# Performance work log

Measured on AMD Instinct MI355X. Metric: run time of the kernel, lower is better.

Reference implementation:

```python
import jax, jax.numpy as jnp
import numpy as np

N_NODES = 100000
N_EDGES = 1600000
D_FEAT = 64
EPS = 1e-07


def setup_inputs() -> dict:
    key = jax.random.key(0)
    k1, k2, k3 = jax.random.split(key, 3)
    x = jax.random.normal(k1, (N_NODES, D_FEAT), dtype=jnp.float32)
    beta = jnp.ones((1,), dtype=jnp.float32)
    edge_row = jnp.sort(jax.random.randint(k2, (N_EDGES,), 0, N_NODES, dtype=jnp.int64))
    edge_col = jax.random.randint(k3, (N_EDGES,), 0, N_NODES, dtype=jnp.int64)
    return {"x": x, "beta": beta, "edge_row": edge_row, "edge_col": edge_col}


def reference(x, beta, edge_row, edge_col):
    # Gather endpoint features: [E, d]
    A = x[edge_row]
    B = x[edge_col]
    # Cosine similarity per edge, scaled by beta: [E]
    inner = jnp.sum(A * B, axis=1)
    norms = jnp.linalg.norm(A, axis=1) * jnp.linalg.norm(B, axis=1)
    sim = beta[0] * (inner / (norms + EPS))
    # Sparse row-wise softmax (tf.sparse.softmax): stable segment softmax over edges grouped by row
    row_max = jax.ops.segment_max(sim, edge_row, num_segments=N_NODES)
    e = jnp.exp(sim - row_max[edge_row])
    row_sum = jax.ops.segment_sum(e, edge_row, num_segments=N_NODES)
    p = e / row_sum[edge_row]  # [E]
    # SPMM: out[i] = sum_{(i,j) in E} p_ij * x[j]
    out = jax.ops.segment_sum(p[:, None] * B, edge_row, num_segments=N_NODES)
    return out
```

## Files before the change

### kernel.cpp

```cpp
#include <hip/hip_runtime.h>
#include <math.h>

#define D_FEAT 64

__global__ __launch_bounds__(256)
void agnn_rnorm(const float* __restrict__ x, float* __restrict__ rn, int n_nodes) {
    int t = blockIdx.x * blockDim.x + threadIdx.x;
    int node = t >> 4;
    if (node >= n_nodes) return;
    int l4 = t & 15;
    float4 v = ((const float4*)x)[node * 16 + l4];
    float ss = v.x * v.x + v.y * v.y + v.z * v.z + v.w * v.w;
    #pragma unroll
    for (int off = 1; off < 16; off <<= 1)
        ss += __shfl_xor(ss, off, 64);
    if (l4 == 0) rn[node] = ss > 0.f ? rsqrtf(ss) : 0.f;
}

__global__ __launch_bounds__(256)
void agnn_rowptr(const int* __restrict__ edge_row, int* __restrict__ row_ptr,
                 int n_nodes, int n_edges) {
    int e = blockIdx.x * blockDim.x + threadIdx.x;
    if (e >= n_edges) return;
    int r1 = edge_row[e];
    int r0 = (e == 0) ? -1 : edge_row[e - 1];
    for (int r = r0 + 1; r <= r1; ++r) row_ptr[r] = e;
    if (e == n_edges - 1) {
        for (int r = r1 + 1; r <= n_nodes; ++r) row_ptr[r] = n_edges;
    }
}

__global__ __launch_bounds__(256)
void agnn_fused(const float* __restrict__ x,
                const float* __restrict__ beta_p,
                const int* __restrict__ edge_col,
                const int* __restrict__ row_ptr,
                const float* __restrict__ rn,
                float* __restrict__ out, int n_nodes) {
    int node = (blockIdx.x * blockDim.x + threadIdx.x) >> 6;
    if (node >= n_nodes) return;
    int lane = threadIdx.x & 63;
    int g  = lane >> 4;
    int l4 = lane & 15;

    const float4* x4 = (const float4*)x;
    float4 xi  = x4[node * 16 + l4];
    float beta = beta_p[0];
    float brni = beta * rn[node];
    float shift = fabsf(beta);

    int es = row_ptr[node];
    int deg = row_ptr[node + 1] - es;

    float s = 0.f;
    float4 acc = {0.f, 0.f, 0.f, 0.f};

    for (int base = 0; base < deg; base += 8) {
        int ei0 = base + g;
        int ei1 = base + 4 + g;
        bool v0 = ei0 < deg;
        bool v1 = ei1 < deg;
        int ea = es + (v0 ? ei0 : 0);
        int eb = es + (v1 ? ei1 : 0);
        int c0 = edge_col[ea];
        int c1 = edge_col[eb];
        float4 a = x4[c0 * 16 + l4];
        float4 b = x4[c1 * 16 + l4];
        float rn0 = rn[c0];
        float rn1 = rn[c1];

        float d0 = a.x * xi.x + a.y * xi.y + a.z * xi.z + a.w * xi.w;
        float d1 = b.x * xi.x + b.y * xi.y + b.z * xi.z + b.w * xi.w;
        #pragma unroll
        for (int off = 1; off < 16; off <<= 1) {
            d0 += __shfl_xor(d0, off, 64);
            d1 += __shfl_xor(d1, off, 64);
        }

        float w0 = v0 ? __expf(brni * d0 * rn0 - shift) : 0.f;
        float w1 = v1 ? __expf(brni * d1 * rn1 - shift) : 0.f;
        s += w0 + w1;
        acc.x += w0 * a.x + w1 * b.x;
        acc.y += w0 * a.y + w1 * b.y;
        acc.z += w0 * a.z + w1 * b.z;
        acc.w += w0 * a.w + w1 * b.w;
    }

    #pragma unroll
    for (int off = 16; off < 64; off <<= 1) {
        s     += __shfl_xor(s,     off, 64);
        acc.x += __shfl_xor(acc.x, off, 64);
        acc.y += __shfl_xor(acc.y, off, 64);
        acc.z += __shfl_xor(acc.z, off, 64);
        acc.w += __shfl_xor(acc.w, off, 64);
    }

    if (g == 0) {
        float inv = (deg > 0 && s > 0.f) ? 1.f / s : 0.f;
        float4 o = {acc.x * inv, acc.y * inv, acc.z * inv, acc.w * inv};
        ((float4*)out)[node * 16 + l4] = o;
    }
}

extern "C" void kernel_launch(void* const* d_in, const int* in_sizes, int n_in,
                              void* d_out, int out_size, void* d_ws, size_t ws_size,
                              hipStream_t stream) {
    const float* x        = (const float*)d_in[0];
    const float* beta     = (const float*)d_in[1];
    const int*   edge_row = (const int*)d_in[2];
    const int*   edge_col = (const int*)d_in[3];
    float* out = (float*)d_out;

    int n_nodes = in_sizes[0] / D_FEAT;
    int n_edges = in_sizes[2];

    float* rn = (float*)d_ws;
    size_t rn_bytes = ((size_t)n_nodes * sizeof(float) + 255) & ~(size_t)255;
    int* row_ptr = (int*)((char*)d_ws + rn_bytes);

    {
        long long threads = (long long)n_nodes * 16;
        int blocks = (int)((threads + 255) / 256);
        agnn_rnorm<<<blocks, 256, 0, stream>>>(x, rn, n_nodes);
    }
    {
        int blocks = (n_edges + 255) / 256;
        agnn_rowptr<<<blocks, 256, 0, stream>>>(edge_row, row_ptr, n_nodes, n_edges);
    }
    {
        int blocks = (n_nodes + 3) / 4;
        agnn_fused<<<blocks, 256, 0, stream>>>(x, beta, edge_col, row_ptr, rn,
                                               out, n_nodes);
    }
}
```

Baseline: 150.3 us.

## Use fp16 MFMA tiles for per-edge scores and SpMM over 16-node tiles

Converts x to an fp16 copy during prep and merges the norm and row_ptr kernels into one launch. The main kernel now gives each wave a tile of 16 consecutive nodes and walks that tile's combined edge list 32 edges at a time. Edge similarities come from MFMA dot products, and the weighted aggregation runs as a second MFMA after staging the gathered features and weights through LDS. Gathered bytes are halved and the shuffle reductions go away, but the MFMA scores are computed against all 16 tile rows and then masked by edge_row, which wastes compute. Inputs and weights are rounded to fp16, which costs precision.

```diff
diff --git a/kernel.cpp b/kernel.cpp
--- a/kernel.cpp
+++ b/kernel.cpp
@@ -2,104 +2,220 @@
 #include <math.h>
 
 #define D_FEAT 64
+#define S_GET(v, i) ((v)[i])
+typedef _Float16 v8h __attribute__((ext_vector_type(8)));
+typedef float v4f __attribute__((ext_vector_type(4)));
+typedef _Float16 h2 __attribute__((ext_vector_type(2)));
+
+__device__ __forceinline__ v8h u2h8(uint4 u) { v8h v; __builtin_memcpy(&v, &u, 16); return v; }
 
 __global__ __launch_bounds__(256)
-void agnn_rnorm(const float* __restrict__ x, float* __restrict__ rn, int n_nodes) {
-    int t = blockIdx.x * blockDim.x + threadIdx.x;
-    int node = t >> 4;
-    if (node >= n_nodes) return;
-    int l4 = t & 15;
-    float4 v = ((const float4*)x)[node * 16 + l4];
-    float ss = v.x * v.x + v.y * v.y + v.z * v.z + v.w * v.w;
-    #pragma unroll
-    for (int off = 1; off < 16; off <<= 1)
-        ss += __shfl_xor(ss, off, 64);
-    if (l4 == 0) rn[node] = ss > 0.f ? rsqrtf(ss) : 0.f;
+void agnn_prep(const float* __restrict__ x, float* __restrict__ rn,
+               uint2* __restrict__ xh, const int* __restrict__ edge_row,
+               int* __restrict__ row_ptr, int n_nodes, int n_edges, int nb_prep) {
+    if ((int)blockIdx.x < nb_prep) {
+        int t = blockIdx.x * blockDim.x + threadIdx.x;
+        int node = t >> 4;
+        if (node >= n_nodes) return;
+        int l4 = t & 15;
+        float4 v = ((const float4*)x)[node * 16 + l4];
+        float ss = v.x*v.x + v.y*v.y + v.z*v.z + v.w*v.w;
+        #pragma unroll
+        for (int off = 1; off < 16; off <<= 1) ss += __shfl_xor(ss, off, 64);
+        if (l4 == 0) rn[node] = ss > 0.f ? rsqrtf(ss) : 0.f;
+        h2 h0 = {(_Float16)v.x, (_Float16)v.y};
+        h2 h1 = {(_Float16)v.z, (_Float16)v.w};
+        uint2 u;
+        __builtin_memcpy(&u.x, &h0, 4);
+        __builtin_memcpy(&u.y, &h1, 4);
+        xh[node * 16 + l4] = u;
+    } else {
+        int e = (blockIdx.x - nb_prep) * blockDim.x + threadIdx.x;
+        if (e >= n_edges) return;
+        int r1 = edge_row[e];
+        int r0 = (e == 0) ? -1 : edge_row[e - 1];
+        for (int r = r0 + 1; r <= r1; ++r) row_ptr[r] = e;
+        if (e == n_edges - 1)
+            for (int r = r1 + 1; r <= n_nodes; ++r) row_ptr[r] = n_edges;
+    }
 }
 
+#define XCP_PITCH 144
+#define P_PITCH    80
+#define WAVE_LDS  (32 * XCP_PITCH + 16 * P_PITCH)
+
 __global__ __launch_bounds__(256)
-void agnn_rowptr(const int* __restrict__ edge_row, int* __restrict__ row_ptr,
-                 int n_nodes, int n_edges) {
-    int e = blockIdx.x * blockDim.x + threadIdx.x;
-    if (e >= n_edges) return;
-    int r1 = edge_row[e];
-    int r0 = (e == 0) ? -1 : edge_row[e - 1];
-    for (int r = r0 + 1; r <= r1; ++r) row_ptr[r] = e;
-    if (e == n_edges - 1) {
-        for (int r = r1 + 1; r <= n_nodes; ++r) row_ptr[r] = n_edges;
-    }
-}
-
-__global__ __launch_bounds__(256)
-void agnn_fused(const float* __restrict__ x,
-                const float* __restrict__ beta_p,
+void agnn_fused(const float* __restrict__ beta_p,
                 const int* __restrict__ edge_col,
+                const int* __restrict__ edge_row,
                 const int* __restrict__ row_ptr,
                 const float* __restrict__ rn,
+                const uint4* __restrict__ xh4,
                 float* __restrict__ out, int n_nodes) {
-    int node = (blockIdx.x * blockDim.x + threadIdx.x) >> 6;
-    if (node >= n_nodes) return;
+    __shared__ char lds_raw[4 * WAVE_LDS];
+    int wid  = threadIdx.x >> 6;
     int lane = threadIdx.x & 63;
-    int g  = lane >> 4;
-    int l4 = lane & 15;
-
-    const float4* x4 = (const float4*)x;
-    float4 xi  = x4[node * 16 + l4];
-    float beta = beta_p[0];
-    float brni = beta * rn[node];
+    int q    = lane >> 4;
+    int lo4  = lane & 15;
+    char* XCP = lds_raw + wid * WAVE_LDS;
+    char* PL  = XCP + 32 * XCP_PITCH;
+
+    int tile = blockIdx.x * 4 + wid;
+    int t0 = tile * 16;
+    if (t0 >= n_nodes) return;
+
+    int qnode = t0 + lo4; if (qnode >= n_nodes) qnode = n_nodes - 1;
+    v8h a0 = u2h8(xh4[(size_t)qnode * 8 + q]);
+    v8h a1 = u2h8(xh4[(size_t)qnode * 8 + 4 + q]);
+
+    float beta  = beta_p[0];
     float shift = fabsf(beta);
-
-    int es = row_ptr[node];
-    int deg = row_ptr[node + 1] - es;
-
-    float s = 0.f;
-    float4 acc = {0.f, 0.f, 0.f, 0.f};
-
-    for (int base = 0; base < deg; base += 8) {
-        int ei0 = base + g;
-        int ei1 = base + 4 + g;
-        bool v0 = ei0 < deg;
-        bool v1 = ei1 < deg;
-        int ea = es + (v0 ? ei0 : 0);
-        int eb = es + (v1 ? ei1 : 0);
-        int c0 = edge_col[ea];
-        int c1 = edge_col[eb];
-        float4 a = x4[c0 * 16 + l4];
-        float4 b = x4[c1 * 16 + l4];
-        float rn0 = rn[c0];
-        float rn1 = rn[c1];
-
-        float d0 = a.x * xi.x + a.y * xi.y + a.z * xi.z + a.w * xi.w;
-        float d1 = b.x * xi.x + b.y * xi.y + b.z * xi.z + b.w * xi.w;
-        #pragma unroll
-        for (int off = 1; off < 16; off <<= 1) {
-            d0 += __shfl_xor(d0, off, 64);
-            d1 += __shfl_xor(d1, off, 64);
-        }
-
-        float w0 = v0 ? __expf(brni * d0 * rn0 - shift) : 0.f;
-        float w1 = v1 ? __expf(brni * d1 * rn1 - shift) : 0.f;
-        s += w0 + w1;
-        acc.x += w0 * a.x + w1 * b.x;
-        acc.y += w0 * a.y + w1 * b.y;
-        acc.z += w0 * a.z + w1 * b.z;
-        acc.w += w0 * a.w + w1 * b.w;
+    float4 rq = *(const float4*)(rn + t0 + q * 4);
+    float brn0 = beta * rq.x, brn1 = beta * rq.y, brn2 = beta * rq.z, brn3 = beta * rq.w;
+
+    int es   = row_ptr[t0];
+    int tend = t0 + 16; if (tend > n_nodes) tend = n_nodes;
+    int L    = row_ptr[tend] - es;
+
+    v4f o0 = {0,0,0,0}, o1 = {0,0,0,0}, o2 = {0,0,0,0}, o3 = {0,0,0,0};
+    float l0 = 0.f, l1 = 0.f, l2 = 0.f, l3 = 0.f;
+    unsigned int selp = (lo4 & 1) ? 0x07060302u : 0x05040100u;
+    int rbase = t0 + q * 4;
+
+    for (int base = 0; base < L; base += 32) {
+        int idx0 = base + lo4;
+        bool cv0 = idx0 < L;
+        int e0 = es + (cv0 ? idx0 : 0);
+        int c0 = edge_col[e0];
+        int rr0 = edge_row[e0];
+        float rnc0 = rn[c0];
+        uint4 u00 = xh4[(size_t)c0 * 8 + q];
+        uint4 u01 = xh4[(size_t)c0 * 8 + 4 + q];
+        int idx1 = base + 16 + lo4;
+        bool cv1 = idx1 < L;
+        int e1 = es + (cv1 ? idx1 : 0);
+        int c1 = edge_col[e1];
+        int rr1 = edge_row[e1];
+        float rnc1 = rn[c1];
+        uint4 u10 = xh4[(size_t)c1 * 8 + q];
+        uint4 u11 = xh4[(size_t)c1 * 8 + 4 + q];
+
+        v4f z0 = {0,0,0,0};
+        z0 = __builtin_amdgcn_mfma_f32_16x16x32_f16(a0, u2h8(u00), z0, 0, 0, 0);
+        z0 = __builtin_amdgcn_mfma_f32_16x16x32_f16(a1, u2h8(u01), z0, 0, 0, 0);
+        v4f z1 = {0,0,0,0};
+        z1 = __builtin_amdgcn_mfma_f32_16x16x32_f16(a0, u2h8(u10), z1, 0, 0, 0);
+        z1 = __builtin_amdgcn_mfma_f32_16x16x32_f16(a1, u2h8(u11), z1, 0, 0, 0);
+
+        {
+            unsigned int colA = lo4 * 4, colB = (16 + lo4) * 4;
+            char* pA = XCP + (4 * q) * XCP_PITCH;
+            char* pB = XCP + (16 + 4 * q) * XCP_PITCH;
+            *(unsigned int*)(pA + 0 * XCP_PITCH + colA) = u00.x;
+            *(unsigned int*)(pA + 1 * XCP_PITCH + colA) = u00.y;
+            *(unsigned int*)(pA + 2 * XCP_PITCH + colA) = u00.z;
+            *(unsigned int*)(pA + 3 * XCP_PITCH + colA) = u00.w;
+            *(unsigned int*)(pB + 0 * XCP_PITCH + colA) = u01.x;
+            *(unsigned int*)(pB + 1 * XCP_PITCH + colA) = u01.y;
+            *(unsigned int*)(pB + 2 * XCP_PITCH + colA) = u01.z;
+            *(unsigned int*)(pB + 3 * XCP_PITCH + colA) = u01.w;
+            *(unsigned int*)(pA + 0 * XCP_PITCH + colB) = u10.x;
+            *(unsigned int*)(pA + 1 * XCP_PITCH + colB) = u10.y;
+            *(unsigned int*)(pA + 2 * XCP_PITCH + colB) = u10.z;
+            *(unsigned int*)(pA + 3 * XCP_PITCH + colB) = u10.w;
+            *(unsigned int*)(pB + 0 * XCP_PITCH + colB) = u11.x;
+            *(unsigned int*)(pB + 1 * XCP_PITCH + colB) = u11.y;
+            *(unsigned int*)(pB + 2 * XCP_PITCH + colB) = u11.z;
+            *(unsigned int*)(pB + 3 * XCP_PITCH + colB) = u11.w;
+        }
+
+        float w00 = (cv0 && rr0 == rbase + 0) ? __expf(brn0 * rnc0 * z0[0] - shift) : 0.f;
+        float w01 = (cv0 && rr0 == rbase + 1) ? __expf(brn1 * rnc0 * z0[1] - shift) : 0.f;
+        float w02 = (cv0 && rr0 == rbase + 2) ? __expf(brn2 * rnc0 * z0[2] - shift) : 0.f;
+        float w03 = (cv0 && rr0 == rbase + 3) ? __expf(brn3 * rnc0 * z0[3] - shift) : 0.f;
+        float w10 = (cv1 && rr1 == rbase + 0) ? __expf(brn0 * rnc1 * z1[0] - shift) : 0.f;
+        float w11 = (cv1 && rr1 == rbase + 1) ? __expf(brn1 * rnc1 * z1[1] - shift) : 0.f;
+        float w12 = (cv1 && rr1 == rbase + 2) ? __expf(brn2 * rnc1 * z1[2] - shift) : 0.f;
+        float w13 = (cv1 && rr1 == rbase + 3) ? __expf(brn3 * rnc1 * z1[3] - shift) : 0.f;
+        l0 += w00 + w10; l1 += w01 + w11; l2 += w02 + w12; l3 += w03 + w13;
+
+        {
+            unsigned int cA = lo4 * 2, cB = (16 + lo4) * 2;
+            char* pm = PL + (q * 4) * P_PITCH;
+            *(_Float16*)(pm + 0 * P_PITCH + cA) = (_Float16)w00;
+            *(_Float16*)(pm + 1 * P_PITCH + cA) = (_Float16)w01;
+            *(_Float16*)(pm + 2 * P_PITCH + cA) = (_Float16)w02;
+            *(_Float16*)(pm + 3 * P_PITCH + cA) = (_Float16)w03;
+            *(_Float16*)(pm + 0 * P_PITCH + cB) = (_Float16)w10;
+            *(_Float16*)(pm + 1 * P_PITCH + cB) = (_Float16)w11;
+            *(_Float16*)(pm + 2 * P_PITCH + cB) = (_Float16)w12;
+            *(_Float16*)(pm + 3 * P_PITCH + cB) = (_Float16)w13;
+        }
+
+        v8h pah = u2h8(*(const uint4*)(PL + lo4 * P_PITCH + q * 16));
+        {
+            const char* rp = XCP + (0 + (lo4 >> 1)) * XCP_PITCH + q * 32;
+            uint4 da = *(const uint4*)rp;
+            uint4 db = *(const uint4*)(rp + 16);
+            uint4 bb = { __builtin_amdgcn_perm(da.y, da.x, selp),
+                         __builtin_amdgcn_perm(da.w, da.z, selp),
+                         __builtin_amdgcn_perm(db.y, db.x, selp),
+                         __builtin_amdgcn_perm(db.w, db.z, selp) };
+            o0 = __builtin_amdgcn_mfma_f32_16x16x32_f16(pah, u2h8(bb), o0, 0, 0, 0);
+        }
+        {
+            const char* rp = XCP + (8 + (lo4 >> 1)) * XCP_PITCH + q * 32;
+            uint4 da = *(const uint4*)rp;
+            uint4 db = *(const uint4*)(rp + 16);
+            uint4 bb = { __builtin_amdgcn_perm(da.y, da.x, selp),
+                         __builtin_amdgcn_perm(da.w, da.z, selp),
+                         __builtin_amdgcn_perm(db.y, db.x, selp),
+                         __builtin_amdgcn_perm(db.w, db.z, selp) };
+            o1 = __builtin_amdgcn_mfma_f32_16x16x32_f16(pah, u2h8(bb), o1, 0, 0, 0);
+        }
+        {
+            const char* rp = XCP + (16 + (lo4 >> 1)) * XCP_PITCH + q * 32;
+            uint4 da = *(const uint4*)rp;
+            uint4 db = *(const uint4*)(rp + 16);
+            uint4 bb = { __builtin_amdgcn_perm(da.y, da.x, selp),
+                         __builtin_amdgcn_perm(da.w, da.z, selp),
+                         __builtin_amdgcn_perm(db.y, db.x, selp),
+                         __builtin_amdgcn_perm(db.w, db.z, selp) };
+            o2 = __builtin_amdgcn_mfma_f32_16x16x32_f16(pah, u2h8(bb), o2, 0, 0, 0);
+        }
+        {
+            const char* rp = XCP + (24 + (lo4 >> 1)) * XCP_PITCH + q * 32;
+            uint4 da = *(const uint4*)rp;
+            uint4 db = *(const uint4*)(rp + 16);
+            uint4 bb = { __builtin_amdgcn_perm(da.y, da.x, selp),
+                         __builtin_amdgcn_perm(da.w, da.z, selp),
+                         __builtin_amdgcn_perm(db.y, db.x, selp),
+                         __builtin_amdgcn_perm(db.w, db.z, selp) };
+            o3 = __builtin_amdgcn_mfma_f32_16x16x32_f16(pah, u2h8(bb), o3, 0, 0, 0);
+        }
     }
 
     #pragma unroll
-    for (int off = 16; off < 64; off <<= 1) {
-        s     += __shfl_xor(s,     off, 64);
-        acc.x += __shfl_xor(acc.x, off, 64);
-        acc.y += __shfl_xor(acc.y, off, 64);
-        acc.z += __shfl_xor(acc.z, off, 64);
-        acc.w += __shfl_xor(acc.w, off, 64);
-    }
-
-    if (g == 0) {
-        float inv = (deg > 0 && s > 0.f) ? 1.f / s : 0.f;
-        float4 o = {acc.x * inv, acc.y * inv, acc.z * inv, acc.w * inv};
-        ((float4*)out)[node * 16 + l4] = o;
-    }
+    for (int off = 1; off < 16; off <<= 1) {
+        l0 += __shfl_xor(l0, off, 64);
+        l1 += __shfl_xor(l1, off, 64);
+        l2 += __shfl_xor(l2, off, 64);
+        l3 += __shfl_xor(l3, off, 64);
+    }
+    float i0 = l0 > 0.f ? 1.f / l0 : 0.f;
+    float i1 = l1 > 0.f ? 1.f / l1 : 0.f;
+    float i2 = l2 > 0.f ? 1.f / l2 : 0.f;
+    float i3 = l3 > 0.f ? 1.f / l3 : 0.f;
+
+    int m0 = rbase;
+    if (m0 + 0 < n_nodes) { float* p = out + (size_t)(m0 + 0) * 64 + lo4;
+        p[0] = o0[0]*i0; p[16] = o1[0]*i0; p[32] = o2[0]*i0; p[48] = o3[0]*i0; }
+    if (m0 + 1 < n_nodes) { float* p = out + (size_t)(m0 + 1) * 64 + lo4;
+        p[0] = o0[1]*i1; p[16] = o1[1]*i1; p[32] = o2[1]*i1; p[48] = o3[1]*i1; }
+    if (m0 + 2 < n_nodes) { float* p = out + (size_t)(m0 + 2) * 64 + lo4;
+        p[0] = o0[2]*i2; p[16] = o1[2]*i2; p[32] = o2[2]*i2; p[48] = o3[2]*i2; }
+    if (m0 + 3 < n_nodes) { float* p = out + (size_t)(m0 + 3) * 64 + lo4;
+        p[0] = o0[3]*i3; p[16] = o1[3]*i3; p[32] = o2[3]*i3; p[48] = o3[3]*i3; }
 }
 
 extern "C" void kernel_launch(void* const* d_in, const int* in_sizes, int n_in,
@@ -114,22 +230,23 @@
     int n_nodes = in_sizes[0] / D_FEAT;
     int n_edges = in_sizes[2];
 
-    float* rn = (float*)d_ws;
-    size_t rn_bytes = ((size_t)n_nodes * sizeof(float) + 255) & ~(size_t)255;
-    int* row_ptr = (int*)((char*)d_ws + rn_bytes);
+    char* ws = (char*)d_ws;
+    float* rn = (float*)ws;
+    size_t off0 = ((size_t)n_nodes * sizeof(float) + 255) & ~(size_t)255;
+    int* row_ptr = (int*)(ws + off0);
+    size_t off1 = off0 + (((size_t)(n_nodes + 1) * sizeof(int) + 255) & ~(size_t)255);
+    uint2* xh = (uint2*)(ws + off1);
 
     {
-        long long threads = (long long)n_nodes * 16;
-        int blocks = (int)((threads + 255) / 256);
-        agnn_rnorm<<<blocks, 256, 0, stream>>>(x, rn, n_nodes);
+        int nb_prep = (n_nodes * 16 + 255) / 256;
+        int nb_rp   = (n_edges + 255) / 256;
+        agnn_prep<<<nb_prep + nb_rp, 256, 0, stream>>>(
+            x, rn, xh, edge_row, row_ptr, n_nodes, n_edges, nb_prep);
     }
     {
-        int blocks = (n_edges + 255) / 256;
-        agnn_rowptr<<<blocks, 256, 0, stream>>>(edge_row, row_ptr, n_nodes, n_edges);
-    }
-    {
-        int blocks = (n_nodes + 3) / 4;
-        agnn_fused<<<blocks, 256, 0, stream>>>(x, beta, edge_col, row_ptr, rn,
-                                               out, n_nodes);
+        int tiles  = (n_nodes + 15) / 16;
+        int blocks = (tiles + 3) / 4;
+        agnn_fused<<<blocks, 256, 0, stream>>>(beta, edge_col, edge_row, row_ptr,
+                                               rn, (const uint4*)xh, out, n_nodes);
     }
 }
```

Result: faster. 130.7 us (-13.0%).
